# Optimization experiments

Hardware: AMD Instinct MI355X
Metric: run time of the kernel (lower is better)

The kernel has to match this reference:

```python
import jax, jax.numpy as jnp
import numpy as np

K = 8
DIM = 64
NUM_BLOCKS = 12
BN_EPS = 1e-5
LRELU_SLOPE = 0.01  # torch nn.LeakyReLU default negative_slope


def knn_indices(xyz, k):
    # xyz: [b, 3, n] -> idx [b, n, k] of k nearest neighbors (self included)
    x = jnp.transpose(xyz, (0, 2, 1))  # [b, n, 3]
    sq = jnp.sum(x * x, axis=-1)  # [b, n]
    d2 = sq[:, :, None] - 2.0 * jnp.einsum('bnd,bmd->bnm', x, x) + sq[:, None, :]
    _, idx = jax.lax.top_k(-d2, k)  # k smallest distances
    return idx


def group_point(points, idx):
    # points [b, d, n], idx [b, n, k] -> grouped [b, d, k, n]
    g = jax.vmap(lambda p, i: p[:, i])(points, idx)  # [b, d, n, k]
    return jnp.transpose(g, (0, 1, 3, 2))


def setup_inputs() -> dict:
    key = jax.random.key(0)
    ks = jax.random.split(key, 6)
    b, n = 8, 4096
    xyz = jax.random.normal(ks[0], (b, 3, n), dtype=jnp.float32)
    points = jax.random.normal(ks[1], (b, DIM, n), dtype=jnp.float32)
    # per-block params (note: the module's second Conv2d per block is never used
    # in forward — layers[4*idx+2] is applied to both center and grouped points)
    conv_w = jax.random.normal(ks[2], (NUM_BLOCKS, DIM, DIM), dtype=jnp.float32) * (1.0 / np.sqrt(DIM))
    conv_b = jax.random.normal(ks[3], (NUM_BLOCKS, DIM), dtype=jnp.float32) * 0.01
    bn_gamma = 1.0 + 0.1 * jax.random.normal(ks[4], (NUM_BLOCKS, DIM), dtype=jnp.float32)
    bn_beta = 0.1 * jax.random.normal(ks[5], (NUM_BLOCKS, DIM), dtype=jnp.float32)
    return {"xyz": xyz, "points": points, "conv_w": conv_w, "conv_b": conv_b,
            "bn_gamma": bn_gamma, "bn_beta": bn_beta}


def reference(xyz, points, conv_w, conv_b, bn_gamma, bn_beta):
    idx = knn_indices(xyz, K)  # fixed graph, computed once in block 0

    def block(p, params):
        w, b, g, be = params  # [DIM,DIM], [DIM], [DIM], [DIM]
        shortcut = p
        # BatchNorm1d (training-mode batch stats over batch & point dims)
        mean = jnp.mean(p, axis=(0, 2), keepdims=True)
        var = jnp.var(p, axis=(0, 2), keepdims=True)
        h = (p - mean) * jax.lax.rsqrt(var + BN_EPS) * g[None, :, None] + be[None, :, None]
        # LeakyReLU
        h = jnp.where(h >= 0, h, LRELU_SLOPE * h)
        # gather neighbor features: [b, d, k, n]
        grouped = group_point(h, idx)
        # shared 1x1 conv on center and grouped points
        center = jnp.einsum('od,bdn->bon', w, h) + b[None, :, None]            # [b,d,n]
        gconv = jnp.einsum('od,bdkn->bokn', w, grouped) + b[None, :, None, None]  # [b,d,k,n]
        # mean over concat([center[:, :, None], gconv], axis=2) == (center + sum_k gconv) / (k+1)
        new_p = (center + jnp.sum(gconv, axis=2)) / (K + 1) + shortcut
        return new_p, None

    out, _ = jax.lax.scan(block, points, (conv_w, conv_b, bn_gamma, bn_beta))
    return out
```

## Files before the change

kernel.cpp:

```cpp
#include <hip/hip_runtime.h>
#include <hip/hip_bf16.h>

#define NB     8
#define NPTS   4096
#define DIMC   64
#define KNN_K  8
#define NBLK   12
#define NREP   8

__global__ __launch_bounds__(256) void prep_kernel(
        const float* __restrict__ xyz, float4* __restrict__ pts4g,
        float* __restrict__ stats) {
#pragma clang fp contract(off)
    int g = blockIdx.x * 256 + threadIdx.x;
    if (g < 13 * NREP * 128) stats[g] = 0.0f;
    int b = g >> 12, j = g & 4095;
    const float* xb = xyz + (size_t)b * 3 * NPTS;
    float x = xb[j];
    float y = xb[NPTS + j];
    float z = xb[2 * NPTS + j];
    float sq = (x * x + y * y) + z * z;
    pts4g[g] = make_float4(x, y, z, sq);
}

__global__ __launch_bounds__(256) void cast_kernel(
        const float* __restrict__ pts,
        float* __restrict__ P0, float* __restrict__ stats0) {
    __shared__ __align__(16) float tr[64 * 65];
    __shared__ float slotA[4 * 64], slotB[4 * 64];
    int wg = blockIdx.x;
    int b = wg & 7;
    int n0 = (wg >> 3) << 6;
    int rep = (wg >> 3) & (NREP - 1);
    int tid = threadIdx.x;
    int lane6 = tid & 63;
    int grp = tid >> 6;

    #pragma unroll
    for (int k = 0; k < 16; ++k) {
        int d = grp + (k << 2);
        float v = pts[(((size_t)((b << 6) + d)) << 12) + n0 + lane6];
        tr[d * 65 + lane6] = v;
    }
    __syncthreads();
    int c = lane6;
    float s = 0.0f, s2 = 0.0f;
    #pragma unroll
    for (int k = 0; k < 16; ++k) {
        int p = grp + (k << 2);
        float v = tr[c * 65 + p];
        P0[((size_t)((b << 12) + n0 + p)) * 64 + c] = v;
        s += v; s2 += v * v;
    }
    slotA[grp * 64 + c] = s;
    slotB[grp * 64 + c] = s2;
    __syncthreads();
    if (tid < 64) {
        float t = slotA[tid] + slotA[64 + tid] + slotA[128 + tid] + slotA[192 + tid];
        atomicAdd(&stats0[rep * 128 + tid], t);
    } else if (tid < 128) {
        int cc = tid - 64;
        float t = slotB[cc] + slotB[64 + cc] + slotB[128 + cc] + slotB[192 + cc];
        atomicAdd(&stats0[rep * 128 + 64 + cc], t);
    }
}

__global__ __launch_bounds__(512) void knn_kernel(
        const float4* __restrict__ pts4g, int* __restrict__ idx) {
#pragma clang fp contract(off)
    __shared__ __align__(16) float4 cand[2048];
    __shared__ double stash[8 * 9 * 64];
    int wg = blockIdx.x;
    int b = wg >> 6;
    int q0 = (wg & 63) << 6;
    int tid = threadIdx.x;

    int lane  = tid & 63;
    int chunk = tid >> 6;

    const float4* cb = pts4g + ((size_t)b << 12);
    float4 qp = cb[q0 + lane];

    double k0, k1, k2, k3, k4, k5, k6, k7;
    k0 = k1 = k2 = k3 = k4 = k5 = k6 = k7 = __builtin_inf();
    float bd7f = 3.4e38f;

    for (int half = 0; half < 2; ++half) {
        if (half) __syncthreads();
        #pragma unroll
        for (int k = 0; k < 4; ++k)
            cand[tid + (k << 9)] = cb[(half << 11) + tid + (k << 9)];
        __syncthreads();

        int jl0 = chunk << 8;
        int jg0 = (half << 11) | jl0;
        for (int jo = 0; jo < 256; jo += 8) {
            float d2v[8];
            #pragma unroll
            for (int u = 0; u < 8; ++u) {
                float4 p = cand[jl0 + jo + u];
                float dot = (qp.x * p.x + qp.y * p.y) + qp.z * p.z;
                d2v[u] = (qp.w - 2.0f * dot) + p.w;
            }
            #pragma unroll
            for (int u = 0; u < 8; ++u) {
                float d2 = d2v[u];
                if (d2 < bd7f) {
                    unsigned long long kb =
                        __double_as_longlong((double)d2) |
                        (unsigned long long)(jg0 + jo + u);
                    double key = __longlong_as_double(kb);
                    double n0 = fmin(k0, key);
                    double n1 = fmin(k1, fmax(k0, key));
                    double n2 = fmin(k2, fmax(k1, key));
                    double n3 = fmin(k3, fmax(k2, key));
                    double n4 = fmin(k4, fmax(k3, key));
                    double n5 = fmin(k5, fmax(k4, key));
                    double n6 = fmin(k6, fmax(k5, key));
                    double n7 = fmin(k7, fmax(k6, key));
                    k0 = n0; k1 = n1; k2 = n2; k3 = n3;
                    k4 = n4; k5 = n5; k6 = n6; k7 = n7;
                    bd7f = (float)k7;
                }
            }
        }
    }

    {
        double* S = &stash[(chunk * 9) * 64 + lane];
        S[0 * 64] = k0; S[1 * 64] = k1; S[2 * 64] = k2; S[3 * 64] = k3;
        S[4 * 64] = k4; S[5 * 64] = k5; S[6 * 64] = k6; S[7 * 64] = k7;
        S[8 * 64] = __builtin_inf();
    }
    __syncthreads();

    if (tid < 64) {
        int h0 = 0, h1 = 0, h2 = 0, h3 = 0, h4 = 0, h5 = 0, h6 = 0, h7 = 0;
        int* op = idx + ((size_t)(b * NPTS + q0 + tid)) * 8;
        #pragma unroll
        for (int t = 0; t < 8; ++t) {
            double v0 = stash[(0 * 9 + h0) * 64 + tid];
            double v1 = stash[(1 * 9 + h1) * 64 + tid];
            double v2 = stash[(2 * 9 + h2) * 64 + tid];
            double v3 = stash[(3 * 9 + h3) * 64 + tid];
            double v4 = stash[(4 * 9 + h4) * 64 + tid];
            double v5 = stash[(5 * 9 + h5) * 64 + tid];
            double v6 = stash[(6 * 9 + h6) * 64 + tid];
            double v7 = stash[(7 * 9 + h7) * 64 + tid];
            double best = v0; int bc = 0;
            if (v1 < best) { best = v1; bc = 1; }
            if (v2 < best) { best = v2; bc = 2; }
            if (v3 < best) { best = v3; bc = 3; }
            if (v4 < best) { best = v4; bc = 4; }
            if (v5 < best) { best = v5; bc = 5; }
            if (v6 < best) { best = v6; bc = 6; }
            if (v7 < best) { best = v7; bc = 7; }
            h0 += (bc == 0); h1 += (bc == 1); h2 += (bc == 2); h3 += (bc == 3);
            h4 += (bc == 4); h5 += (bc == 5); h6 += (bc == 6); h7 += (bc == 7);
            op[t] = (int)(__double_as_longlong(best) & 0xFFFULL);
        }
    }
}

__global__ __launch_bounds__(512) void block_kernel(
        const float* __restrict__ Pin, float* __restrict__ Pout,
        const float* __restrict__ statsIn, float* __restrict__ statsOut,
        const float* __restrict__ Wp, const float* __restrict__ Bp,
        const float* __restrict__ Gp, const float* __restrict__ Betap,
        const int* __restrict__ gidx, float* __restrict__ dout, int last) {
    __shared__ __align__(16) float Wt[64 * 68];
    __shared__ __align__(16) float mt[64 * 68];
    __shared__ __align__(16) float selft[64 * 64];
    __shared__ __align__(16) int   idxl[64 * 8];
    __shared__ __align__(16) float scale_l[64], shift_l[64], bias_l[64];
    __shared__ float slot[8 * 128];

    int wg = blockIdx.x;
    int b = wg & 7;
    int n0 = (wg >> 3) << 6;
    int rep = (wg >> 3) & (NREP - 1);
    int tid = threadIdx.x;

    const float* Pb = Pin + (((size_t)b) << 18);

    if (tid < 128) {
        ((int4*)idxl)[tid] = ((const int4*)(gidx + ((size_t)(b * NPTS + n0)) * 8))[tid];
    }
    #pragma unroll
    for (int k = 0; k < 2; ++k) {
        int lin = tid + (k << 9);
        ((float4*)selft)[lin] = ((const float4*)&Pb[(size_t)n0 << 6])[lin];
    }
    #pragma unroll
    for (int k = 0; k < 8; ++k) {
        int lin = tid + (k << 9);
        int o = lin >> 6, d = lin & 63;
        Wt[d * 68 + o] = Wp[lin];
    }
    if (tid < 64) {
        int c = tid;
        float sum = 0.0f, sumsq = 0.0f;
        #pragma unroll
        for (int r = 0; r < NREP; ++r) {
            sum   += statsIn[r * 128 + c];
            sumsq += statsIn[r * 128 + 64 + c];
        }
        float mean = sum * (1.0f / 32768.0f);
        float var  = sumsq * (1.0f / 32768.0f) - mean * mean;
        float rs   = 1.0f / sqrtf(var + 1e-5f);
        float sc   = Gp[c] * rs;
        scale_l[c] = sc;
        shift_l[c] = Betap[c] - mean * sc;
        bias_l[c]  = Bp[c];
    }
    __syncthreads();

    {
        int cq = tid & 15;
        int pp = tid >> 4;
        int c4 = cq << 2;
        float4 sc4 = *(const float4*)&scale_l[c4];
        float4 sh4 = *(const float4*)&shift_l[c4];
        #pragma unroll
        for (int i = 0; i < 2; ++i) {
            int pt = (pp << 1) + i;
            int4 ja = *(const int4*)&idxl[pt * 8];
            int4 jb = *(const int4*)&idxl[pt * 8 + 4];
            float4 v[9];
            v[0] = *(const float4*)&selft[(pt << 6) + c4];
            v[1] = *(const float4*)&Pb[(((size_t)ja.x) << 6) + c4];
            v[2] = *(const float4*)&Pb[(((size_t)ja.y) << 6) + c4];
            v[3] = *(const float4*)&Pb[(((size_t)ja.z) << 6) + c4];
            v[4] = *(const float4*)&Pb[(((size_t)ja.w) << 6) + c4];
            v[5] = *(const float4*)&Pb[(((size_t)jb.x) << 6) + c4];
            v[6] = *(const float4*)&Pb[(((size_t)jb.y) << 6) + c4];
            v[7] = *(const float4*)&Pb[(((size_t)jb.z) << 6) + c4];
            v[8] = *(const float4*)&Pb[(((size_t)jb.w) << 6) + c4];
            float4 a = make_float4(0.f, 0.f, 0.f, 0.f);
            #pragma unroll
            for (int k = 0; k < 9; ++k) {
                float hx = v[k].x * sc4.x + sh4.x;
                float hy = v[k].y * sc4.y + sh4.y;
                float hz = v[k].z * sc4.z + sh4.z;
                float hw = v[k].w * sc4.w + sh4.w;
                a.x += fmaxf(hx, 0.01f * hx);
                a.y += fmaxf(hy, 0.01f * hy);
                a.z += fmaxf(hz, 0.01f * hz);
                a.w += fmaxf(hw, 0.01f * hw);
            }
            mt[(c4 + 0) * 68 + pt] = a.x * (1.0f / 9.0f);
            mt[(c4 + 1) * 68 + pt] = a.y * (1.0f / 9.0f);
            mt[(c4 + 2) * 68 + pt] = a.z * (1.0f / 9.0f);
            mt[(c4 + 3) * 68 + pt] = a.w * (1.0f / 9.0f);
        }
    }
    __syncthreads();

    int o0 = (tid & 15) << 2;
    int p0 = (tid >> 4) << 1;
    float4 acc[2];
    {
        float4 bias4 = *(const float4*)&bias_l[o0];
        acc[0] = bias4; acc[1] = bias4;
    }
    #pragma unroll
    for (int d = 0; d < 64; ++d) {
        float4 wv = *(const float4*)&Wt[d * 68 + o0];
        float2 a  = *(const float2*)&mt[d * 68 + p0];
        acc[0].x += wv.x * a.x; acc[0].y += wv.y * a.x; acc[0].z += wv.z * a.x; acc[0].w += wv.w * a.x;
        acc[1].x += wv.x * a.y; acc[1].y += wv.y * a.y; acc[1].z += wv.z * a.y; acc[1].w += wv.w * a.y;
    }

    #pragma unroll
    for (int j = 0; j < 2; ++j) {
        float4 r = *(const float4*)&selft[((p0 + j) << 6) + o0];
        acc[j].x += r.x; acc[j].y += r.y; acc[j].z += r.z; acc[j].w += r.w;
    }

    if (!last) {
        float* PbOut = Pout + ((((size_t)b) << 12) + n0) * 64;
        #pragma unroll
        for (int j = 0; j < 2; ++j)
            *(float4*)&PbOut[((size_t)(p0 + j)) * 64 + o0] = acc[j];

        float4 s, s2;
        s.x = acc[0].x + acc[1].x;  s.y = acc[0].y + acc[1].y;
        s.z = acc[0].z + acc[1].z;  s.w = acc[0].w + acc[1].w;
        s2.x = acc[0].x*acc[0].x + acc[1].x*acc[1].x;
        s2.y = acc[0].y*acc[0].y + acc[1].y*acc[1].y;
        s2.z = acc[0].z*acc[0].z + acc[1].z*acc[1].z;
        s2.w = acc[0].w*acc[0].w + acc[1].w*acc[1].w;
        #pragma unroll
        for (int m = 16; m <= 32; m <<= 1) {
            s.x += __shfl_xor(s.x, m, 64);  s.y += __shfl_xor(s.y, m, 64);
            s.z += __shfl_xor(s.z, m, 64);  s.w += __shfl_xor(s.w, m, 64);
            s2.x += __shfl_xor(s2.x, m, 64); s2.y += __shfl_xor(s2.y, m, 64);
            s2.z += __shfl_xor(s2.z, m, 64); s2.w += __shfl_xor(s2.w, m, 64);
        }
        if ((tid & 63) < 16) {
            int w = tid >> 6;
            slot[w * 128 + o0 + 0] = s.x;  slot[w * 128 + o0 + 1] = s.y;
            slot[w * 128 + o0 + 2] = s.z;  slot[w * 128 + o0 + 3] = s.w;
            slot[w * 128 + 64 + o0 + 0] = s2.x; slot[w * 128 + 64 + o0 + 1] = s2.y;
            slot[w * 128 + 64 + o0 + 2] = s2.z; slot[w * 128 + 64 + o0 + 3] = s2.w;
        }
        __syncthreads();
        if (tid < 128) {
            float t = 0.0f;
            #pragma unroll
            for (int w = 0; w < 8; ++w) t += slot[w * 128 + tid];
            atomicAdd(&statsOut[rep * 128 + tid], t);
        }
    } else {
        __syncthreads();
        float* stage = mt;
        #pragma unroll
        for (int j = 0; j < 2; ++j) {
            stage[(o0 + 0) * 64 + p0 + j] = acc[j].x;
            stage[(o0 + 1) * 64 + p0 + j] = acc[j].y;
            stage[(o0 + 2) * 64 + p0 + j] = acc[j].z;
            stage[(o0 + 3) * 64 + p0 + j] = acc[j].w;
        }
        __syncthreads();
        #pragma unroll
        for (int k = 0; k < 8; ++k) {
            int lin = tid + (k << 9);
            int o = lin >> 6, pt = lin & 63;
            dout[(((size_t)((b << 6) + o)) << 12) + n0 + pt] = stage[lin];
        }
    }
}

extern "C" void kernel_launch(void* const* d_in, const int* in_sizes, int n_in,
                              void* d_out, int out_size, void* d_ws, size_t ws_size,
                              hipStream_t stream) {
    const float* xyz    = (const float*)d_in[0];
    const float* pts    = (const float*)d_in[1];
    const float* conv_w = (const float*)d_in[2];
    const float* conv_b = (const float*)d_in[3];
    const float* gamma  = (const float*)d_in[4];
    const float* beta   = (const float*)d_in[5];
    float* out = (float*)d_out;

    char* ws = (char*)d_ws;
    float*  P0    = (float*)(ws);
    float*  P1    = (float*)(ws + (size_t)8 * 1024 * 1024);
    int*    idx   = (int*)  (ws + (size_t)16 * 1024 * 1024);
    float*  stats = (float*)(ws + (size_t)17 * 1024 * 1024);
    float4* pts4g = (float4*)(ws + (size_t)18 * 1024 * 1024);

    prep_kernel<<<128, 256, 0, stream>>>(xyz, pts4g, stats);
    cast_kernel<<<512, 256, 0, stream>>>(pts, P0, stats);
    knn_kernel<<<512, 512, 0, stream>>>(pts4g, idx);

    float* Pbuf[2] = {P0, P1};
    for (int t = 0; t < NBLK; ++t) {
        block_kernel<<<512, 512, 0, stream>>>(
            Pbuf[t & 1], Pbuf[(t + 1) & 1],
            stats + (size_t)t * NREP * 128, stats + (size_t)(t + 1) * NREP * 128,
            conv_w + (size_t)t * 4096, conv_b + (size_t)t * 64,
            gamma + (size_t)t * 64, beta + (size_t)t * 64,
            idx, out, (t == NBLK - 1) ? 1 : 0);
    }
}
```

Baseline: 336.0 us.

## Two-pass float kNN with threshold recollection; drop block kernel LDS staging

The kNN kernel now runs its per-thread top-8 insertion network in float instead of packed double keys. It then merges to find the 8th-smallest distance per query and does a second distance pass that collects candidates at or below that threshold into LDS via atomics, sorting up to 16 with their indices. The block kernel drops the self-tile, index and scale/shift LDS staging: each thread loads its own indices and stats and computes BN scale/shift in registers, and the residual comes from the loaded self vector. This trades a second distance sweep for cheaper float compares, and ties beyond 16 candidates would be truncated.

```diff
diff --git a/kernel.cpp b/kernel.cpp
--- a/kernel.cpp
+++ b/kernel.cpp
@@ -69,21 +69,24 @@
         const float4* __restrict__ pts4g, int* __restrict__ idx) {
 #pragma clang fp contract(off)
     __shared__ __align__(16) float4 cand[2048];
-    __shared__ double stash[8 * 9 * 64];
+    __shared__ float stashv[8 * 9 * 64];
+    __shared__ double colK[64 * 17];
+    __shared__ float v8s[64];
+    __shared__ int   cnts[64];
+
     int wg = blockIdx.x;
     int b = wg >> 6;
     int q0 = (wg & 63) << 6;
     int tid = threadIdx.x;
-
     int lane  = tid & 63;
     int chunk = tid >> 6;
 
     const float4* cb = pts4g + ((size_t)b << 12);
     float4 qp = cb[q0 + lane];
 
-    double k0, k1, k2, k3, k4, k5, k6, k7;
-    k0 = k1 = k2 = k3 = k4 = k5 = k6 = k7 = __builtin_inf();
-    float bd7f = 3.4e38f;
+    float k0, k1, k2, k3, k4, k5, k6, k7;
+    k0 = k1 = k2 = k3 = k4 = k5 = k6 = k7 = __builtin_inff();
+    float gate = __builtin_inff();
 
     for (int half = 0; half < 2; ++half) {
         if (half) __syncthreads();
@@ -93,7 +96,6 @@
         __syncthreads();
 
         int jl0 = chunk << 8;
-        int jg0 = (half << 11) | jl0;
         for (int jo = 0; jo < 256; jo += 8) {
             float d2v[8];
             #pragma unroll
@@ -105,58 +107,102 @@
             #pragma unroll
             for (int u = 0; u < 8; ++u) {
                 float d2 = d2v[u];
-                if (d2 < bd7f) {
-                    unsigned long long kb =
-                        __double_as_longlong((double)d2) |
-                        (unsigned long long)(jg0 + jo + u);
-                    double key = __longlong_as_double(kb);
-                    double n0 = fmin(k0, key);
-                    double n1 = fmin(k1, fmax(k0, key));
-                    double n2 = fmin(k2, fmax(k1, key));
-                    double n3 = fmin(k3, fmax(k2, key));
-                    double n4 = fmin(k4, fmax(k3, key));
-                    double n5 = fmin(k5, fmax(k4, key));
-                    double n6 = fmin(k6, fmax(k5, key));
-                    double n7 = fmin(k7, fmax(k6, key));
+                if (d2 < gate) {
+                    float n0 = fminf(k0, d2);
+                    float n1 = fminf(k1, fmaxf(k0, d2));
+                    float n2 = fminf(k2, fmaxf(k1, d2));
+                    float n3 = fminf(k3, fmaxf(k2, d2));
+                    float n4 = fminf(k4, fmaxf(k3, d2));
+                    float n5 = fminf(k5, fmaxf(k4, d2));
+                    float n6 = fminf(k6, fmaxf(k5, d2));
+                    float n7 = fminf(k7, fmaxf(k6, d2));
                     k0 = n0; k1 = n1; k2 = n2; k3 = n3;
                     k4 = n4; k5 = n5; k6 = n6; k7 = n7;
-                    bd7f = (float)k7;
+                    gate = k7;
                 }
             }
         }
     }
-
     {
-        double* S = &stash[(chunk * 9) * 64 + lane];
+        float* S = &stashv[(chunk * 9) * 64 + lane];
         S[0 * 64] = k0; S[1 * 64] = k1; S[2 * 64] = k2; S[3 * 64] = k3;
         S[4 * 64] = k4; S[5 * 64] = k5; S[6 * 64] = k6; S[7 * 64] = k7;
-        S[8 * 64] = __builtin_inf();
+        S[8 * 64] = __builtin_inff();
     }
     __syncthreads();
 
     if (tid < 64) {
         int h0 = 0, h1 = 0, h2 = 0, h3 = 0, h4 = 0, h5 = 0, h6 = 0, h7 = 0;
-        int* op = idx + ((size_t)(b * NPTS + q0 + tid)) * 8;
+        float v = 0.0f;
         #pragma unroll
         for (int t = 0; t < 8; ++t) {
-            double v0 = stash[(0 * 9 + h0) * 64 + tid];
-            double v1 = stash[(1 * 9 + h1) * 64 + tid];
-            double v2 = stash[(2 * 9 + h2) * 64 + tid];
-            double v3 = stash[(3 * 9 + h3) * 64 + tid];
-            double v4 = stash[(4 * 9 + h4) * 64 + tid];
-            double v5 = stash[(5 * 9 + h5) * 64 + tid];
-            double v6 = stash[(6 * 9 + h6) * 64 + tid];
-            double v7 = stash[(7 * 9 + h7) * 64 + tid];
-            double best = v0; int bc = 0;
-            if (v1 < best) { best = v1; bc = 1; }
-            if (v2 < best) { best = v2; bc = 2; }
-            if (v3 < best) { best = v3; bc = 3; }
-            if (v4 < best) { best = v4; bc = 4; }
-            if (v5 < best) { best = v5; bc = 5; }
-            if (v6 < best) { best = v6; bc = 6; }
-            if (v7 < best) { best = v7; bc = 7; }
+            float x;
+            v = stashv[(0 * 9 + h0) * 64 + tid]; int bc = 0;
+            x = stashv[(1 * 9 + h1) * 64 + tid]; if (x < v) { v = x; bc = 1; }
+            x = stashv[(2 * 9 + h2) * 64 + tid]; if (x < v) { v = x; bc = 2; }
+            x = stashv[(3 * 9 + h3) * 64 + tid]; if (x < v) { v = x; bc = 3; }
+            x = stashv[(4 * 9 + h4) * 64 + tid]; if (x < v) { v = x; bc = 4; }
+            x = stashv[(5 * 9 + h5) * 64 + tid]; if (x < v) { v = x; bc = 5; }
+            x = stashv[(6 * 9 + h6) * 64 + tid]; if (x < v) { v = x; bc = 6; }
+            x = stashv[(7 * 9 + h7) * 64 + tid]; if (x < v) { v = x; bc = 7; }
             h0 += (bc == 0); h1 += (bc == 1); h2 += (bc == 2); h3 += (bc == 3);
             h4 += (bc == 4); h5 += (bc == 5); h6 += (bc == 6); h7 += (bc == 7);
+        }
+        v8s[tid] = v;
+        cnts[tid] = 0;
+    }
+    __syncthreads();
+
+    float v8 = v8s[lane];
+    for (int half = 0; half < 2; ++half) {
+        #pragma unroll
+        for (int k = 0; k < 4; ++k)
+            cand[tid + (k << 9)] = cb[(half << 11) + tid + (k << 9)];
+        __syncthreads();
+        int jl0 = chunk << 8;
+        int jg0 = (half << 11) | jl0;
+        for (int jo = 0; jo < 256; jo += 8) {
+            float d2v[8];
+            #pragma unroll
+            for (int u = 0; u < 8; ++u) {
+                float4 p = cand[jl0 + jo + u];
+                float dot = (qp.x * p.x + qp.y * p.y) + qp.z * p.z;
+                d2v[u] = (qp.w - 2.0f * dot) + p.w;
+            }
+            #pragma unroll
+            for (int u = 0; u < 8; ++u) {
+                if (d2v[u] <= v8) {
+                    int pos = atomicAdd(&cnts[lane], 1);
+                    if (pos < 16) {
+                        unsigned long long kb =
+                            __double_as_longlong((double)d2v[u]) |
+                            (unsigned long long)(jg0 + jo + u);
+                        colK[lane * 17 + pos] = __longlong_as_double(kb);
+                    }
+                }
+            }
+        }
+        __syncthreads();
+    }
+
+    if (tid < 64) {
+        int n = cnts[tid]; if (n > 16) n = 16;
+        double a[16];
+        #pragma unroll
+        for (int i = 0; i < 16; ++i)
+            a[i] = (i < n) ? colK[tid * 17 + i] : __builtin_inf();
+        int* op = idx + ((size_t)(b * NPTS + q0 + tid)) * 8;
+        unsigned used = 0;
+        #pragma unroll
+        for (int t = 0; t < 8; ++t) {
+            double best = __builtin_inf(); int bm = 0;
+            #pragma unroll
+            for (int i = 0; i < 16; ++i) {
+                bool ok = (((used >> i) & 1u) == 0u) && (a[i] < best);
+                best = ok ? a[i] : best;
+                bm   = ok ? i : bm;
+            }
+            used |= 1u << bm;
             op[t] = (int)(__double_as_longlong(best) & 0xFFFULL);
         }
     }
@@ -170,9 +216,6 @@
         const int* __restrict__ gidx, float* __restrict__ dout, int last) {
     __shared__ __align__(16) float Wt[64 * 68];
     __shared__ __align__(16) float mt[64 * 68];
-    __shared__ __align__(16) float selft[64 * 64];
-    __shared__ __align__(16) int   idxl[64 * 8];
-    __shared__ __align__(16) float scale_l[64], shift_l[64], bias_l[64];
     __shared__ float slot[8 * 128];
 
     int wg = blockIdx.x;
@@ -183,84 +226,88 @@
 
     const float* Pb = Pin + (((size_t)b) << 18);
 
-    if (tid < 128) {
-        ((int4*)idxl)[tid] = ((const int4*)(gidx + ((size_t)(b * NPTS + n0)) * 8))[tid];
-    }
-    #pragma unroll
-    for (int k = 0; k < 2; ++k) {
-        int lin = tid + (k << 9);
-        ((float4*)selft)[lin] = ((const float4*)&Pb[(size_t)n0 << 6])[lin];
-    }
+    int cq = tid & 15, c4 = cq << 2;
+    int pp = tid >> 4;
+    int pt0 = pp << 1;
+
+    const int* gp0 = gidx + ((size_t)(b * NPTS + n0 + pt0)) * 8;
+    int4 ja0 = *(const int4*)(gp0);
+    int4 jb0 = *(const int4*)(gp0 + 4);
+    int4 ja1 = *(const int4*)(gp0 + 8);
+    int4 jb1 = *(const int4*)(gp0 + 12);
+
+    float4 sum4 = make_float4(0.f, 0.f, 0.f, 0.f);
+    float4 sq4  = make_float4(0.f, 0.f, 0.f, 0.f);
+    #pragma unroll
+    for (int r = 0; r < NREP; ++r) {
+        float4 s = *(const float4*)&statsIn[r * 128 + c4];
+        float4 q = *(const float4*)&statsIn[r * 128 + 64 + c4];
+        sum4.x += s.x; sum4.y += s.y; sum4.z += s.z; sum4.w += s.w;
+        sq4.x  += q.x; sq4.y  += q.y; sq4.z  += q.z; sq4.w  += q.w;
+    }
+    float4 g4  = *(const float4*)&Gp[c4];
+    float4 be4 = *(const float4*)&Betap[c4];
+    float4 sc4, sh4;
+    {
+        float mean, var, rs;
+        mean = sum4.x * (1.0f / 32768.0f); var = sq4.x * (1.0f / 32768.0f) - mean * mean;
+        rs = 1.0f / sqrtf(var + 1e-5f); sc4.x = g4.x * rs; sh4.x = be4.x - mean * sc4.x;
+        mean = sum4.y * (1.0f / 32768.0f); var = sq4.y * (1.0f / 32768.0f) - mean * mean;
+        rs = 1.0f / sqrtf(var + 1e-5f); sc4.y = g4.y * rs; sh4.y = be4.y - mean * sc4.y;
+        mean = sum4.z * (1.0f / 32768.0f); var = sq4.z * (1.0f / 32768.0f) - mean * mean;
+        rs = 1.0f / sqrtf(var + 1e-5f); sc4.z = g4.z * rs; sh4.z = be4.z - mean * sc4.z;
+        mean = sum4.w * (1.0f / 32768.0f); var = sq4.w * (1.0f / 32768.0f) - mean * mean;
+        rs = 1.0f / sqrtf(var + 1e-5f); sc4.w = g4.w * rs; sh4.w = be4.w - mean * sc4.w;
+    }
+
     #pragma unroll
     for (int k = 0; k < 8; ++k) {
         int lin = tid + (k << 9);
         int o = lin >> 6, d = lin & 63;
         Wt[d * 68 + o] = Wp[lin];
     }
-    if (tid < 64) {
-        int c = tid;
-        float sum = 0.0f, sumsq = 0.0f;
-        #pragma unroll
-        for (int r = 0; r < NREP; ++r) {
-            sum   += statsIn[r * 128 + c];
-            sumsq += statsIn[r * 128 + 64 + c];
-        }
-        float mean = sum * (1.0f / 32768.0f);
-        float var  = sumsq * (1.0f / 32768.0f) - mean * mean;
-        float rs   = 1.0f / sqrtf(var + 1e-5f);
-        float sc   = Gp[c] * rs;
-        scale_l[c] = sc;
-        shift_l[c] = Betap[c] - mean * sc;
-        bias_l[c]  = Bp[c];
+
+    float4 res[2];
+    #pragma unroll
+    for (int i = 0; i < 2; ++i) {
+        int pt = pt0 + i;
+        int4 ja = i ? ja1 : ja0;
+        int4 jb = i ? jb1 : jb0;
+        float4 v[9];
+        v[0] = *(const float4*)&Pb[(((size_t)(n0 + pt)) << 6) + c4];
+        v[1] = *(const float4*)&Pb[(((size_t)ja.x) << 6) + c4];
+        v[2] = *(const float4*)&Pb[(((size_t)ja.y) << 6) + c4];
+        v[3] = *(const float4*)&Pb[(((size_t)ja.z) << 6) + c4];
+        v[4] = *(const float4*)&Pb[(((size_t)ja.w) << 6) + c4];
+        v[5] = *(const float4*)&Pb[(((size_t)jb.x) << 6) + c4];
+        v[6] = *(const float4*)&Pb[(((size_t)jb.y) << 6) + c4];
+        v[7] = *(const float4*)&Pb[(((size_t)jb.z) << 6) + c4];
+        v[8] = *(const float4*)&Pb[(((size_t)jb.w) << 6) + c4];
+        res[i] = v[0];
+        float4 a = make_float4(0.f, 0.f, 0.f, 0.f);
+        #pragma unroll
+        for (int k = 0; k < 9; ++k) {
+            float hx = v[k].x * sc4.x + sh4.x;
+            float hy = v[k].y * sc4.y + sh4.y;
+            float hz = v[k].z * sc4.z + sh4.z;
+            float hw = v[k].w * sc4.w + sh4.w;
+            a.x += fmaxf(hx, 0.01f * hx);
+            a.y += fmaxf(hy, 0.01f * hy);
+            a.z += fmaxf(hz, 0.01f * hz);
+            a.w += fmaxf(hw, 0.01f * hw);
+        }
+        mt[(c4 + 0) * 68 + pt] = a.x * (1.0f / 9.0f);
+        mt[(c4 + 1) * 68 + pt] = a.y * (1.0f / 9.0f);
+        mt[(c4 + 2) * 68 + pt] = a.z * (1.0f / 9.0f);
+        mt[(c4 + 3) * 68 + pt] = a.w * (1.0f / 9.0f);
     }
     __syncthreads();
 
-    {
-        int cq = tid & 15;
-        int pp = tid >> 4;
-        int c4 = cq << 2;
-        float4 sc4 = *(const float4*)&scale_l[c4];
-        float4 sh4 = *(const float4*)&shift_l[c4];
-        #pragma unroll
-        for (int i = 0; i < 2; ++i) {
-            int pt = (pp << 1) + i;
-            int4 ja = *(const int4*)&idxl[pt * 8];
-            int4 jb = *(const int4*)&idxl[pt * 8 + 4];
-            float4 v[9];
-            v[0] = *(const float4*)&selft[(pt << 6) + c4];
-            v[1] = *(const float4*)&Pb[(((size_t)ja.x) << 6) + c4];
-            v[2] = *(const float4*)&Pb[(((size_t)ja.y) << 6) + c4];
-            v[3] = *(const float4*)&Pb[(((size_t)ja.z) << 6) + c4];
-            v[4] = *(const float4*)&Pb[(((size_t)ja.w) << 6) + c4];
-            v[5] = *(const float4*)&Pb[(((size_t)jb.x) << 6) + c4];
-            v[6] = *(const float4*)&Pb[(((size_t)jb.y) << 6) + c4];
-            v[7] = *(const float4*)&Pb[(((size_t)jb.z) << 6) + c4];
-            v[8] = *(const float4*)&Pb[(((size_t)jb.w) << 6) + c4];
-            float4 a = make_float4(0.f, 0.f, 0.f, 0.f);
-            #pragma unroll
-            for (int k = 0; k < 9; ++k) {
-                float hx = v[k].x * sc4.x + sh4.x;
-                float hy = v[k].y * sc4.y + sh4.y;
-                float hz = v[k].z * sc4.z + sh4.z;
-                float hw = v[k].w * sc4.w + sh4.w;
-                a.x += fmaxf(hx, 0.01f * hx);
-                a.y += fmaxf(hy, 0.01f * hy);
-                a.z += fmaxf(hz, 0.01f * hz);
-                a.w += fmaxf(hw, 0.01f * hw);
-            }
-            mt[(c4 + 0) * 68 + pt] = a.x * (1.0f / 9.0f);
-            mt[(c4 + 1) * 68 + pt] = a.y * (1.0f / 9.0f);
-            mt[(c4 + 2) * 68 + pt] = a.z * (1.0f / 9.0f);
-            mt[(c4 + 3) * 68 + pt] = a.w * (1.0f / 9.0f);
-        }
-    }
-    __syncthreads();
-
-    int o0 = (tid & 15) << 2;
-    int p0 = (tid >> 4) << 1;
+    int o0 = c4;
+    int p0 = pt0;
     float4 acc[2];
     {
-        float4 bias4 = *(const float4*)&bias_l[o0];
+        float4 bias4 = *(const float4*)&Bp[o0];
         acc[0] = bias4; acc[1] = bias4;
     }
     #pragma unroll
@@ -273,8 +320,8 @@
 
     #pragma unroll
     for (int j = 0; j < 2; ++j) {
-        float4 r = *(const float4*)&selft[((p0 + j) << 6) + o0];
-        acc[j].x += r.x; acc[j].y += r.y; acc[j].z += r.z; acc[j].w += r.w;
+        acc[j].x += res[j].x; acc[j].y += res[j].y;
+        acc[j].z += res[j].z; acc[j].w += res[j].w;
     }
 
     if (!last) {
```

New measurement: 374.9 us. +11.6%, slower.
